# Performance work log

Hardware: AMD Instinct MI355X
Metric: run time of the kernel (lower is better)

The kernel has to match this reference:

```python
import jax, jax.numpy as jnp
import numpy as np

S = 512      # num_seg (queries)
T = 16384    # frames
D = 512      # d_model
DFF = 2048   # dim_feedforward
EPS = 1e-5


def layer_norm(x, g, b):
    mu = jnp.mean(x, axis=-1, keepdims=True)
    var = jnp.mean((x - mu) ** 2, axis=-1, keepdims=True)
    return (x - mu) * jax.lax.rsqrt(var + EPS) * g + b


def setup_inputs() -> dict:
    key = jax.random.key(0)
    ks = jax.random.split(key, 16)
    inv = 1.0 / np.sqrt(D)
    invf = 1.0 / np.sqrt(DFF)
    # action_idx: exactly S contiguous segments over T frames
    action_idx = (jnp.arange(T, dtype=jnp.int32) * S) // T
    return {
        "tgt": jax.random.normal(ks[0], (S, 1, D), jnp.float32),
        "memory": jax.random.normal(ks[1], (T, 1, D), jnp.float32),
        "pos": jax.random.normal(ks[2], (T, 1, D), jnp.float32),
        "query_pos": jax.random.normal(ks[3], (S, 1, D), jnp.float32),
        "action_idx": action_idx,
        "W_tgt2": jax.random.uniform(ks[4], (D, D), jnp.float32, -inv, inv),
        "b_tgt2": jax.random.uniform(ks[5], (D,), jnp.float32, -inv, inv),
        "W1": jax.random.uniform(ks[6], (DFF, D), jnp.float32, -inv, inv),
        "b1": jax.random.uniform(ks[7], (DFF,), jnp.float32, -inv, inv),
        "W2": jax.random.uniform(ks[8], (D, DFF), jnp.float32, -invf, invf),
        "b2": jax.random.uniform(ks[9], (D,), jnp.float32, -invf, invf),
        "g2": jnp.ones((D,), jnp.float32),
        "be2": jnp.zeros((D,), jnp.float32),
        "g3": jnp.ones((D,), jnp.float32),
        "be3": jnp.zeros((D,), jnp.float32),
    }


def reference(tgt, memory, pos, query_pos, action_idx,
              W_tgt2, b_tgt2, W1, b1, W2, b2, g2, be2, g3, be3):
    num_seg, _, dim = tgt.shape
    q = tgt + query_pos          # [S, 1, D]
    k = memory + pos             # [T, 1, D]
    v = memory                   # [T, 1, D]

    # segment-neighbor mask: seg_id per frame; query s attends to frames in
    # segments {s-1, s, s+1}
    change = jnp.concatenate([jnp.zeros((1,), jnp.int32),
                              (action_idx[1:] != action_idx[:-1]).astype(jnp.int32)])
    seg_id = jnp.cumsum(change)                                   # [T]
    mask = jnp.abs(seg_id[None, :] - jnp.arange(num_seg)[:, None]) <= 1  # [S, T]

    scores = jnp.einsum("sbd,tbd->bst", q, k) / np.sqrt(dim)      # [1, S, T]
    scores = jnp.where(mask[None], scores, -jnp.inf)
    attn = jax.nn.softmax(scores, axis=-1)                        # [1, S, T]

    ctx = jnp.einsum("bst,tbd->sbd", attn, v)                     # [S, 1, D]
    tgt2 = jax.nn.relu(ctx) @ W_tgt2.T + b_tgt2                   # [S, 1, D]
    x = layer_norm(tgt + tgt2, g2, be2)
    ffn = jax.nn.relu(x @ W1.T + b1) @ W2.T + b2
    out = layer_norm(x + ffn, g3, be3)
    return out
```

## Files before the change

kernel.cpp:

```cpp
#include <hip/hip_runtime.h>
#include <math.h>

#define S_Q  512
#define T_F  16384
#define D_M  512
#define DFF_ 2048
#define SEG  32

typedef __attribute__((ext_vector_type(8))) short short8;
typedef __attribute__((ext_vector_type(4))) float floatx4;

__device__ __forceinline__ unsigned short f2bf(float f) {
    unsigned int u = __builtin_bit_cast(unsigned int, f);
    u += 0x7FFFu + ((u >> 16) & 1u);
    return (unsigned short)(u >> 16);
}

__device__ __forceinline__ void async_copy16(const void* g, void* l) {
    __builtin_amdgcn_global_load_lds(
        (const __attribute__((address_space(1))) void*)g,
        (__attribute__((address_space(3))) void*)l, 16, 0, 0);
}

__global__ __launch_bounds__(256) void conv3_bf16(
    const float* __restrict__ w0, unsigned short* __restrict__ o0, int n0,
    const float* __restrict__ w1, unsigned short* __restrict__ o1, int n1,
    const float* __restrict__ w2, unsigned short* __restrict__ o2)
{
    int i = (blockIdx.x * 256 + threadIdx.x) * 4;
    const float* src; unsigned short* dst;
    if (i < n0)            { src = w0; dst = o0; }
    else if (i < n0 + n1)  { src = w1; dst = o1; i -= n0; }
    else                   { src = w2; dst = o2; i -= n0 + n1; }
    const float4 v = *(const float4*)(src + i);
    unsigned short o[4] = {f2bf(v.x), f2bf(v.y), f2bf(v.z), f2bf(v.w)};
    *(uint2*)(dst + i) = *(const uint2*)o;
}

__global__ __launch_bounds__(256) void attn_kernel(
    const float* __restrict__ tgt, const float* __restrict__ memory,
    const float* __restrict__ pos, const float* __restrict__ query_pos,
    unsigned short* __restrict__ rc)
{
    const int b    = blockIdx.x;
    const int s    = (b & 7) * 64 + (b >> 3);
    const int tid  = threadIdx.x;
    const int lane = tid & 63;
    const int wave = tid >> 6;

    __shared__ float q[D_M];
    __shared__ float sc[96];

    for (int d = tid; d < D_M; d += 256)
        q[d] = tgt[s * D_M + d] + query_pos[s * D_M + d];
    __syncthreads();

    int lo = (s - 1) * SEG; if (lo < 0) lo = 0;
    int hi = (s + 2) * SEG; if (hi > T_F) hi = T_F;
    const int nf = hi - lo;

    const float4* q4 = (const float4*)q;
    #pragma unroll 2
    for (int f = wave; f < nf; f += 4) {
        const float4* m4 = (const float4*)(memory + (size_t)(lo + f) * D_M);
        const float4* p4 = (const float4*)(pos    + (size_t)(lo + f) * D_M);
        float acc = 0.f;
        #pragma unroll
        for (int j = 0; j < 2; ++j) {
            const int idx = lane + 64 * j;
            const float4 qq = q4[idx], mm = m4[idx], pp = p4[idx];
            acc += qq.x * (mm.x + pp.x) + qq.y * (mm.y + pp.y)
                 + qq.z * (mm.z + pp.z) + qq.w * (mm.w + pp.w);
        }
        #pragma unroll
        for (int off = 32; off > 0; off >>= 1)
            acc += __shfl_xor(acc, off, 64);
        if (lane == 0) sc[f] = acc * 0.04419417382415922f;
    }
    __syncthreads();

    float m = -1e30f;
    for (int f = 0; f < nf; ++f) m = fmaxf(m, sc[f]);
    __syncthreads();
    for (int f = tid; f < nf; f += 256) sc[f] = __expf(sc[f] - m);
    __syncthreads();
    float denom = 0.f;
    for (int f = 0; f < nf; ++f) denom += sc[f];
    const float inv = 1.f / denom;

    float ax = 0.f, ay = 0.f;
    const int d0 = tid * 2;
    #pragma unroll 4
    for (int f = 0; f < nf; ++f) {
        const float a = sc[f];
        const float2 v = *(const float2*)(memory + (size_t)(lo + f) * D_M + d0);
        ax += a * v.x; ay += a * v.y;
    }
    const unsigned short o0 = f2bf(fmaxf(ax * inv, 0.f));
    const unsigned short o1 = f2bf(fmaxf(ay * inv, 0.f));
    *(unsigned int*)(rc + (size_t)s * D_M + d0) = (unsigned int)o0 | ((unsigned int)o1 << 16);
}

template<int BM, bool RELU, bool ADDRES, bool OUT_BF16>
__global__ __launch_bounds__(256) void gemm_mfma(
    const unsigned short* __restrict__ A,
    const unsigned short* __restrict__ B,
    const float* __restrict__ bias,
    const float* __restrict__ res,
    void* __restrict__ Cout, int M, int N, int K)
{
    constexpr int BK = 64;
    constexpr int WT = BM / 2;
    constexpr int NT = WT / 16;
    constexpr int NR = BM / 32;
    __shared__ short As[BM * BK];
    __shared__ short Bs[BM * BK];

    const int tid  = threadIdx.x;
    const int lane = tid & 63;
    const int wave = tid >> 6;
    const int m0 = blockIdx.y * BM;
    const int n0 = blockIdx.x * BM;

    const int srow = tid >> 3;
    const int scol = (tid & 7) * 8;
    const int quad = lane >> 4;
    const int r16  = lane & 15;
    const int wm = (wave >> 1) * WT;
    const int wn = (wave & 1) * WT;

    floatx4 acc[NT][NT] = {};

    for (int k0 = 0; k0 < K; k0 += BK) {
        #pragma unroll
        for (int r = 0; r < NR; ++r) {
            async_copy16(A + (size_t)(m0 + r * 32 + srow) * K + k0 + scol,
                         As + r * 2048 + wave * 512);
            async_copy16(B + (size_t)(n0 + r * 32 + srow) * K + k0 + scol,
                         Bs + r * 2048 + wave * 512);
        }
        __syncthreads();
        #pragma unroll
        for (int ks = 0; ks < 2; ++ks) {
            short8 a[NT], bb[NT];
            #pragma unroll
            for (int i = 0; i < NT; ++i) {
                a[i]  = *(const short8*)(As + (wm + i * 16 + r16) * BK + ks * 32 + quad * 8);
                bb[i] = *(const short8*)(Bs + (wn + i * 16 + r16) * BK + ks * 32 + quad * 8);
            }
            #pragma unroll
            for (int i = 0; i < NT; ++i)
                #pragma unroll
                for (int j = 0; j < NT; ++j)
                    acc[i][j] = __builtin_amdgcn_mfma_f32_16x16x32_bf16(a[i], bb[j], acc[i][j], 0, 0, 0);
        }
        __syncthreads();
    }

    #pragma unroll
    for (int nj = 0; nj < NT; ++nj) {
        const int col = n0 + wn + nj * 16 + r16;
        const float bs = bias[col];
        #pragma unroll
        for (int mi = 0; mi < NT; ++mi) {
            #pragma unroll
            for (int r = 0; r < 4; ++r) {
                const int row = m0 + wm + mi * 16 + quad * 4 + r;
                float c = acc[mi][nj][r] + bs;
                if (RELU)   c = fmaxf(c, 0.f);
                if (ADDRES) c += res[(size_t)row * N + col];
                if (OUT_BF16)
                    ((unsigned short*)Cout)[(size_t)row * N + col] = f2bf(c);
                else
                    ((float*)Cout)[(size_t)row * N + col] = c;
            }
        }
    }
}

template<bool WRITE_BF16>
__global__ __launch_bounds__(256) void ln_kernel(
    const float* __restrict__ X, const float* __restrict__ g,
    const float* __restrict__ be, float* __restrict__ out,
    unsigned short* __restrict__ out_bf)
{
    const int row  = blockIdx.x * 4 + (threadIdx.x >> 6);
    const int lane = threadIdx.x & 63;
    const float* x = X + (size_t)row * D_M;

    float v[8];
    float sum = 0.f;
    #pragma unroll
    for (int j = 0; j < 8; ++j) { v[j] = x[lane + 64 * j]; sum += v[j]; }
    #pragma unroll
    for (int off = 32; off > 0; off >>= 1) sum += __shfl_xor(sum, off, 64);
    const float mu = sum * (1.0f / 512.0f);

    float var = 0.f;
    #pragma unroll
    for (int j = 0; j < 8; ++j) { const float d = v[j] - mu; var += d * d; }
    #pragma unroll
    for (int off = 32; off > 0; off >>= 1) var += __shfl_xor(var, off, 64);
    const float r = rsqrtf(var * (1.0f / 512.0f) + 1e-5f);

    #pragma unroll
    for (int j = 0; j < 8; ++j) {
        const int d = lane + 64 * j;
        const float o = (v[j] - mu) * r * g[d] + be[d];
        out[(size_t)row * D_M + d] = o;
        if (WRITE_BF16) out_bf[(size_t)row * D_M + d] = f2bf(o);
    }
}

extern "C" void kernel_launch(void* const* d_in, const int* in_sizes, int n_in,
                              void* d_out, int out_size, void* d_ws, size_t ws_size,
                              hipStream_t stream) {
    const float* tgt       = (const float*)d_in[0];
    const float* memory    = (const float*)d_in[1];
    const float* pos       = (const float*)d_in[2];
    const float* query_pos = (const float*)d_in[3];
    const float* W_tgt2 = (const float*)d_in[5];
    const float* b_tgt2 = (const float*)d_in[6];
    const float* W1     = (const float*)d_in[7];
    const float* b1     = (const float*)d_in[8];
    const float* W2     = (const float*)d_in[9];
    const float* b2     = (const float*)d_in[10];
    const float* g2     = (const float*)d_in[11];
    const float* be2    = (const float*)d_in[12];
    const float* g3     = (const float*)d_in[13];
    const float* be3    = (const float*)d_in[14];
    float* out = (float*)d_out;

    char* w = (char*)d_ws;
    unsigned short* rc  = (unsigned short*)w;  w += (size_t)S_Q * D_M * 2;
    float* y            = (float*)w;           w += (size_t)S_Q * D_M * 4;
    float* x            = (float*)w;           w += (size_t)S_Q * D_M * 4;
    unsigned short* xb  = (unsigned short*)w;  w += (size_t)S_Q * D_M * 2;
    unsigned short* h   = (unsigned short*)w;  w += (size_t)S_Q * DFF_ * 2;
    float* y2           = (float*)w;           w += (size_t)S_Q * D_M * 4;
    unsigned short* Wt2b= (unsigned short*)w;  w += (size_t)D_M * D_M * 2;
    unsigned short* W1b = (unsigned short*)w;  w += (size_t)DFF_ * D_M * 2;
    unsigned short* W2b = (unsigned short*)w;  w += (size_t)D_M * DFF_ * 2;

    conv3_bf16<<<(D_M * D_M + DFF_ * D_M + D_M * DFF_) / 1024, 256, 0, stream>>>(
        W_tgt2, Wt2b, D_M * D_M, W1, W1b, DFF_ * D_M, W2, W2b);

    attn_kernel<<<S_Q, 256, 0, stream>>>(tgt, memory, pos, query_pos, rc);

    gemm_mfma<32, false, true, false><<<dim3(D_M / 32, S_Q / 32), 256, 0, stream>>>(
        rc, Wt2b, b_tgt2, tgt, y, S_Q, D_M, D_M);
    ln_kernel<true><<<S_Q / 4, 256, 0, stream>>>(y, g2, be2, x, xb);
    gemm_mfma<64, true, false, true><<<dim3(DFF_ / 64, S_Q / 64), 256, 0, stream>>>(
        xb, W1b, b1, nullptr, h, S_Q, DFF_, D_M);
    gemm_mfma<32, false, true, false><<<dim3(D_M / 32, S_Q / 32), 256, 0, stream>>>(
        h, W2b, b2, x, y2, S_Q, D_M, DFF_);
    ln_kernel<false><<<S_Q / 4, 256, 0, stream>>>(y2, g3, be3, out, nullptr);
}
```

Baseline: 192.1 us.

## Restructure attention per segment, add split-K GEMMs, double buffering, fused LN merge

Attention now runs one block per key segment. Each block loads the segment's memory into LDS once and computes partial softmax statistics and context for the three neighbouring queries, so memory and pos are no longer re-read three times. A merge kernel combines the partials with a log-sum-exp rescale. The GEMMs gain double-buffered LDS staging, and the two narrow GEMMs use split-K to expose more blocks. Bias, residual and partial reduction move into the layernorm kernels. The cost is an extra kernel launch and extra workspace traffic for the partials.

```diff
diff --git a/kernel.cpp b/kernel.cpp
--- a/kernel.cpp
+++ b/kernel.cpp
@@ -6,6 +6,7 @@
 #define D_M  512
 #define DFF_ 2048
 #define SEG  32
+#define SCALE 0.04419417382415922f
 
 typedef __attribute__((ext_vector_type(8))) short short8;
 typedef __attribute__((ext_vector_type(4))) float floatx4;
@@ -37,90 +38,166 @@
     *(uint2*)(dst + i) = *(const uint2*)o;
 }
 
-__global__ __launch_bounds__(256) void attn_kernel(
+__global__ __launch_bounds__(256) void attn_seg(
     const float* __restrict__ tgt, const float* __restrict__ memory,
-    const float* __restrict__ pos, const float* __restrict__ query_pos,
-    unsigned short* __restrict__ rc)
-{
-    const int b    = blockIdx.x;
-    const int s    = (b & 7) * 64 + (b >> 3);
+    const float* __restrict__ pos, const float* __restrict__ qp,
+    float* __restrict__ part,
+    float2* __restrict__ me)
+{
+    const int j    = blockIdx.x;
     const int tid  = threadIdx.x;
     const int lane = tid & 63;
     const int wave = tid >> 6;
 
-    __shared__ float q[D_M];
-    __shared__ float sc[96];
-
-    for (int d = tid; d < D_M; d += 256)
-        q[d] = tgt[s * D_M + d] + query_pos[s * D_M + d];
+    __shared__ float v[SEG * D_M];
+    __shared__ float sc[3][SEG];
+    __shared__ float pr[3][SEG];
+
+    {
+        const float* g = memory + (size_t)j * SEG * D_M + (size_t)wave * 16 * 256 + lane * 4;
+        #pragma unroll
+        for (int r = 0; r < 16; ++r)
+            async_copy16(g + r * 256, v + (wave * 16 + r) * 256);
+    }
+
+    float q0[8] = {}, q1[8] = {}, q2[8] = {};
+    {
+        const int d = lane * 8;
+        if (j > 0) {
+            const float4 a0 = *(const float4*)(tgt + (size_t)(j - 1) * D_M + d);
+            const float4 a1 = *(const float4*)(tgt + (size_t)(j - 1) * D_M + d + 4);
+            const float4 b0 = *(const float4*)(qp  + (size_t)(j - 1) * D_M + d);
+            const float4 b1 = *(const float4*)(qp  + (size_t)(j - 1) * D_M + d + 4);
+            q0[0]=a0.x+b0.x; q0[1]=a0.y+b0.y; q0[2]=a0.z+b0.z; q0[3]=a0.w+b0.w;
+            q0[4]=a1.x+b1.x; q0[5]=a1.y+b1.y; q0[6]=a1.z+b1.z; q0[7]=a1.w+b1.w;
+        }
+        {
+            const float4 a0 = *(const float4*)(tgt + (size_t)j * D_M + d);
+            const float4 a1 = *(const float4*)(tgt + (size_t)j * D_M + d + 4);
+            const float4 b0 = *(const float4*)(qp  + (size_t)j * D_M + d);
+            const float4 b1 = *(const float4*)(qp  + (size_t)j * D_M + d + 4);
+            q1[0]=a0.x+b0.x; q1[1]=a0.y+b0.y; q1[2]=a0.z+b0.z; q1[3]=a0.w+b0.w;
+            q1[4]=a1.x+b1.x; q1[5]=a1.y+b1.y; q1[6]=a1.z+b1.z; q1[7]=a1.w+b1.w;
+        }
+        if (j < S_Q - 1) {
+            const float4 a0 = *(const float4*)(tgt + (size_t)(j + 1) * D_M + d);
+            const float4 a1 = *(const float4*)(tgt + (size_t)(j + 1) * D_M + d + 4);
+            const float4 b0 = *(const float4*)(qp  + (size_t)(j + 1) * D_M + d);
+            const float4 b1 = *(const float4*)(qp  + (size_t)(j + 1) * D_M + d + 4);
+            q2[0]=a0.x+b0.x; q2[1]=a0.y+b0.y; q2[2]=a0.z+b0.z; q2[3]=a0.w+b0.w;
+            q2[4]=a1.x+b1.x; q2[5]=a1.y+b1.y; q2[6]=a1.z+b1.z; q2[7]=a1.w+b1.w;
+        }
+    }
     __syncthreads();
 
-    int lo = (s - 1) * SEG; if (lo < 0) lo = 0;
-    int hi = (s + 2) * SEG; if (hi > T_F) hi = T_F;
-    const int nf = hi - lo;
-
-    const float4* q4 = (const float4*)q;
-    #pragma unroll 2
-    for (int f = wave; f < nf; f += 4) {
-        const float4* m4 = (const float4*)(memory + (size_t)(lo + f) * D_M);
-        const float4* p4 = (const float4*)(pos    + (size_t)(lo + f) * D_M);
-        float acc = 0.f;
-        #pragma unroll
-        for (int j = 0; j < 2; ++j) {
-            const int idx = lane + 64 * j;
-            const float4 qq = q4[idx], mm = m4[idx], pp = p4[idx];
-            acc += qq.x * (mm.x + pp.x) + qq.y * (mm.y + pp.y)
-                 + qq.z * (mm.z + pp.z) + qq.w * (mm.w + pp.w);
-        }
-        #pragma unroll
-        for (int off = 32; off > 0; off >>= 1)
-            acc += __shfl_xor(acc, off, 64);
-        if (lane == 0) sc[f] = acc * 0.04419417382415922f;
+    #pragma unroll
+    for (int r = 0; r < 8; ++r) {
+        const int f = wave * 8 + r;
+        const size_t t = (size_t)(j * SEG + f);
+        const float4 pA = *(const float4*)(pos + t * D_M + lane * 8);
+        const float4 pB = *(const float4*)(pos + t * D_M + lane * 8 + 4);
+        const float4 mA = *(const float4*)(v + f * D_M + lane * 8);
+        const float4 mB = *(const float4*)(v + f * D_M + lane * 8 + 4);
+        const float k8[8] = {mA.x+pA.x, mA.y+pA.y, mA.z+pA.z, mA.w+pA.w,
+                             mB.x+pB.x, mB.y+pB.y, mB.z+pB.z, mB.w+pB.w};
+        float a0 = 0.f, a1 = 0.f, a2 = 0.f;
+        #pragma unroll
+        for (int i = 0; i < 8; ++i) {
+            a0 += k8[i] * q0[i]; a1 += k8[i] * q1[i]; a2 += k8[i] * q2[i];
+        }
+        #pragma unroll
+        for (int off = 32; off > 0; off >>= 1) {
+            a0 += __shfl_xor(a0, off, 64);
+            a1 += __shfl_xor(a1, off, 64);
+            a2 += __shfl_xor(a2, off, 64);
+        }
+        if (lane == 0) { sc[0][f] = a0 * SCALE; sc[1][f] = a1 * SCALE; sc[2][f] = a2 * SCALE; }
     }
     __syncthreads();
 
-    float m = -1e30f;
-    for (int f = 0; f < nf; ++f) m = fmaxf(m, sc[f]);
+    if (wave < 3) {
+        float mx = -1e30f;
+        for (int f = 0; f < SEG; ++f) mx = fmaxf(mx, sc[wave][f]);
+        float e = 0.f;
+        for (int f = 0; f < SEG; ++f) {
+            const float pe = __expf(sc[wave][f] - mx);
+            e += pe;
+            if (lane == 0) pr[wave][f] = pe;
+        }
+        const int q = j - 1 + wave;
+        if (lane == 0 && q >= 0 && q < S_Q)
+            me[q * 3 + (2 - wave)] = make_float2(mx, e);
+    }
     __syncthreads();
-    for (int f = tid; f < nf; f += 256) sc[f] = __expf(sc[f] - m);
-    __syncthreads();
-    float denom = 0.f;
-    for (int f = 0; f < nf; ++f) denom += sc[f];
-    const float inv = 1.f / denom;
-
-    float ax = 0.f, ay = 0.f;
+
     const int d0 = tid * 2;
-    #pragma unroll 4
-    for (int f = 0; f < nf; ++f) {
-        const float a = sc[f];
-        const float2 v = *(const float2*)(memory + (size_t)(lo + f) * D_M + d0);
-        ax += a * v.x; ay += a * v.y;
-    }
-    const unsigned short o0 = f2bf(fmaxf(ax * inv, 0.f));
-    const unsigned short o1 = f2bf(fmaxf(ay * inv, 0.f));
-    *(unsigned int*)(rc + (size_t)s * D_M + d0) = (unsigned int)o0 | ((unsigned int)o1 << 16);
-}
-
-template<int BM, bool RELU, bool ADDRES, bool OUT_BF16>
+    float c0x=0,c0y=0,c1x=0,c1y=0,c2x=0,c2y=0;
+    for (int f = 0; f < SEG; ++f) {
+        const float2 vv = *(const float2*)(v + f * D_M + d0);
+        const float w0 = pr[0][f], w1 = pr[1][f], w2 = pr[2][f];
+        c0x += w0 * vv.x; c0y += w0 * vv.y;
+        c1x += w1 * vv.x; c1y += w1 * vv.y;
+        c2x += w2 * vv.x; c2y += w2 * vv.y;
+    }
+    if (j > 0)
+        *(float2*)(part + ((size_t)(j - 1) * 3 + 2) * D_M + d0) = make_float2(c0x, c0y);
+    *(float2*)(part + ((size_t)j * 3 + 1) * D_M + d0) = make_float2(c1x, c1y);
+    if (j < S_Q - 1)
+        *(float2*)(part + ((size_t)(j + 1) * 3 + 0) * D_M + d0) = make_float2(c2x, c2y);
+}
+
+__global__ __launch_bounds__(256) void attn_merge(
+    const float* __restrict__ part, const float2* __restrict__ me,
+    unsigned short* __restrict__ rc)
+{
+    const int row  = blockIdx.x * 4 + (threadIdx.x >> 6);
+    const int lane = threadIdx.x & 63;
+    const int slo = (row == 0)       ? 1 : 0;
+    const int shi = (row == S_Q - 1) ? 1 : 2;
+
+    float mx = -1e30f;
+    for (int s = slo; s <= shi; ++s) mx = fmaxf(mx, me[row * 3 + s].x);
+    float den = 0.f, c[3] = {0.f, 0.f, 0.f};
+    for (int s = slo; s <= shi; ++s) {
+        c[s] = __expf(me[row * 3 + s].x - mx);
+        den += me[row * 3 + s].y * c[s];
+    }
+    const float inv = 1.f / den;
+
+    const int d = lane * 8;
+    float acc[8] = {};
+    for (int s = slo; s <= shi; ++s) {
+        const float4 a = *(const float4*)(part + ((size_t)row * 3 + s) * D_M + d);
+        const float4 b = *(const float4*)(part + ((size_t)row * 3 + s) * D_M + d + 4);
+        acc[0]+=c[s]*a.x; acc[1]+=c[s]*a.y; acc[2]+=c[s]*a.z; acc[3]+=c[s]*a.w;
+        acc[4]+=c[s]*b.x; acc[5]+=c[s]*b.y; acc[6]+=c[s]*b.z; acc[7]+=c[s]*b.w;
+    }
+    unsigned short o[8];
+    #pragma unroll
+    for (int i = 0; i < 8; ++i) o[i] = f2bf(fmaxf(acc[i] * inv, 0.f));
+    *(uint4*)(rc + (size_t)row * D_M + d) = *(const uint4*)o;
+}
+
+template<int BM, int KSPLIT, bool RELU, bool ADDRES, bool OUT_BF16>
 __global__ __launch_bounds__(256) void gemm_mfma(
-    const unsigned short* __restrict__ A,
-    const unsigned short* __restrict__ B,
-    const float* __restrict__ bias,
-    const float* __restrict__ res,
+    const unsigned short* __restrict__ A, const unsigned short* __restrict__ B,
+    const float* __restrict__ bias, const float* __restrict__ res,
     void* __restrict__ Cout, int M, int N, int K)
 {
     constexpr int BK = 64;
     constexpr int WT = BM / 2;
     constexpr int NT = WT / 16;
     constexpr int NR = BM / 32;
-    __shared__ short As[BM * BK];
-    __shared__ short Bs[BM * BK];
+    __shared__ short As[2][BM * BK];
+    __shared__ short Bs[2][BM * BK];
 
     const int tid  = threadIdx.x;
     const int lane = tid & 63;
     const int wave = tid >> 6;
     const int m0 = blockIdx.y * BM;
     const int n0 = blockIdx.x * BM;
+    const int kbase = (K / KSPLIT) * blockIdx.z;
+    const int niter = (K / KSPLIT) / BK;
 
     const int srow = tid >> 3;
     const int scol = (tid & 7) * 8;
@@ -131,84 +208,121 @@
 
     floatx4 acc[NT][NT] = {};
 
-    for (int k0 = 0; k0 < K; k0 += BK) {
-        #pragma unroll
-        for (int r = 0; r < NR; ++r) {
-            async_copy16(A + (size_t)(m0 + r * 32 + srow) * K + k0 + scol,
-                         As + r * 2048 + wave * 512);
-            async_copy16(B + (size_t)(n0 + r * 32 + srow) * K + k0 + scol,
-                         Bs + r * 2048 + wave * 512);
-        }
+    #pragma unroll
+    for (int r = 0; r < NR; ++r) {
+        async_copy16(A + (size_t)(m0 + r * 32 + srow) * K + kbase + scol, &As[0][r * 2048 + wave * 512]);
+        async_copy16(B + (size_t)(n0 + r * 32 + srow) * K + kbase + scol, &Bs[0][r * 2048 + wave * 512]);
+    }
+
+    for (int it = 0; it < niter; ++it) {
         __syncthreads();
+        if (it + 1 < niter) {
+            const int k0 = kbase + (it + 1) * BK;
+            const int nb = (it + 1) & 1;
+            #pragma unroll
+            for (int r = 0; r < NR; ++r) {
+                async_copy16(A + (size_t)(m0 + r * 32 + srow) * K + k0 + scol, &As[nb][r * 2048 + wave * 512]);
+                async_copy16(B + (size_t)(n0 + r * 32 + srow) * K + k0 + scol, &Bs[nb][r * 2048 + wave * 512]);
+            }
+        }
+        const short* Ab = As[it & 1];
+        const short* Bb = Bs[it & 1];
         #pragma unroll
         for (int ks = 0; ks < 2; ++ks) {
             short8 a[NT], bb[NT];
             #pragma unroll
             for (int i = 0; i < NT; ++i) {
-                a[i]  = *(const short8*)(As + (wm + i * 16 + r16) * BK + ks * 32 + quad * 8);
-                bb[i] = *(const short8*)(Bs + (wn + i * 16 + r16) * BK + ks * 32 + quad * 8);
+                a[i]  = *(const short8*)(Ab + (wm + i * 16 + r16) * BK + ks * 32 + quad * 8);
+                bb[i] = *(const short8*)(Bb + (wn + i * 16 + r16) * BK + ks * 32 + quad * 8);
             }
             #pragma unroll
             for (int i = 0; i < NT; ++i)
                 #pragma unroll
-                for (int j = 0; j < NT; ++j)
-                    acc[i][j] = __builtin_amdgcn_mfma_f32_16x16x32_bf16(a[i], bb[j], acc[i][j], 0, 0, 0);
-        }
-        __syncthreads();
+                for (int jn = 0; jn < NT; ++jn)
+                    acc[i][jn] = __builtin_amdgcn_mfma_f32_16x16x32_bf16(a[i], bb[jn], acc[i][jn], 0, 0, 0);
+        }
     }
 
     #pragma unroll
     for (int nj = 0; nj < NT; ++nj) {
         const int col = n0 + wn + nj * 16 + r16;
-        const float bs = bias[col];
         #pragma unroll
         for (int mi = 0; mi < NT; ++mi) {
             #pragma unroll
             for (int r = 0; r < 4; ++r) {
                 const int row = m0 + wm + mi * 16 + quad * 4 + r;
-                float c = acc[mi][nj][r] + bs;
-                if (RELU)   c = fmaxf(c, 0.f);
-                if (ADDRES) c += res[(size_t)row * N + col];
-                if (OUT_BF16)
-                    ((unsigned short*)Cout)[(size_t)row * N + col] = f2bf(c);
-                else
-                    ((float*)Cout)[(size_t)row * N + col] = c;
+                float cv = acc[mi][nj][r];
+                if (KSPLIT > 1) {
+                    ((float*)Cout)[((size_t)blockIdx.z * M + row) * N + col] = cv;
+                } else {
+                    cv += bias[col];
+                    if (RELU)   cv = fmaxf(cv, 0.f);
+                    if (ADDRES) cv += res[(size_t)row * N + col];
+                    if (OUT_BF16)
+                        ((unsigned short*)Cout)[(size_t)row * N + col] = f2bf(cv);
+                    else
+                        ((float*)Cout)[(size_t)row * N + col] = cv;
+                }
             }
         }
     }
 }
 
-template<bool WRITE_BF16>
-__global__ __launch_bounds__(256) void ln_kernel(
-    const float* __restrict__ X, const float* __restrict__ g,
-    const float* __restrict__ be, float* __restrict__ out,
-    unsigned short* __restrict__ out_bf)
+template<int NP, bool WRITE_BF16>
+__global__ __launch_bounds__(256) void ln_merge(
+    const float* __restrict__ parts,
+    const float* __restrict__ res, const float* __restrict__ bias,
+    const float* __restrict__ g, const float* __restrict__ be,
+    float* __restrict__ out, unsigned short* __restrict__ out_bf)
 {
     const int row  = blockIdx.x * 4 + (threadIdx.x >> 6);
     const int lane = threadIdx.x & 63;
-    const float* x = X + (size_t)row * D_M;
-
-    float v[8];
+
+    float vv[8];
+    #pragma unroll
+    for (int hh = 0; hh < 2; ++hh) {
+        const int d = lane * 8 + hh * 4;
+        float4 a = *(const float4*)(res + (size_t)row * D_M + d);
+        const float4 b = *(const float4*)(bias + d);
+        a.x += b.x; a.y += b.y; a.z += b.z; a.w += b.w;
+        #pragma unroll
+        for (int z = 0; z < NP; ++z) {
+            const float4 p = *(const float4*)(parts + ((size_t)z * S_Q + row) * D_M + d);
+            a.x += p.x; a.y += p.y; a.z += p.z; a.w += p.w;
+        }
+        vv[hh * 4 + 0] = a.x; vv[hh * 4 + 1] = a.y;
+        vv[hh * 4 + 2] = a.z; vv[hh * 4 + 3] = a.w;
+    }
+
     float sum = 0.f;
     #pragma unroll
-    for (int j = 0; j < 8; ++j) { v[j] = x[lane + 64 * j]; sum += v[j]; }
+    for (int i = 0; i < 8; ++i) sum += vv[i];
     #pragma unroll
     for (int off = 32; off > 0; off >>= 1) sum += __shfl_xor(sum, off, 64);
     const float mu = sum * (1.0f / 512.0f);
 
     float var = 0.f;
     #pragma unroll
-    for (int j = 0; j < 8; ++j) { const float d = v[j] - mu; var += d * d; }
+    for (int i = 0; i < 8; ++i) { const float dd = vv[i] - mu; var += dd * dd; }
     #pragma unroll
     for (int off = 32; off > 0; off >>= 1) var += __shfl_xor(var, off, 64);
-    const float r = rsqrtf(var * (1.0f / 512.0f) + 1e-5f);
-
-    #pragma unroll
-    for (int j = 0; j < 8; ++j) {
-        const int d = lane + 64 * j;
-        const float o = (v[j] - mu) * r * g[d] + be[d];
-        out[(size_t)row * D_M + d] = o;
-        if (WRITE_BF16) out_bf[(size_t)row * D_M + d] = f2bf(o);
+    const float rr = rsqrtf(var * (1.0f / 512.0f) + 1e-5f);
+
+    #pragma unroll
+    for (int hh = 0; hh < 2; ++hh) {
+        const int d = lane * 8 + hh * 4;
+        const float4 gg = *(const float4*)(g + d);
+        const float4 bb = *(const float4*)(be + d);
+        float4 o;
+        o.x = (vv[hh*4+0] - mu) * rr * gg.x + bb.x;
+        o.y = (vv[hh*4+1] - mu) * rr * gg.y + bb.y;
+        o.z = (vv[hh*4+2] - mu) * rr * gg.z + bb.z;
+        o.w = (vv[hh*4+3] - mu) * rr * gg.w + bb.w;
+        *(float4*)(out + (size_t)row * D_M + d) = o;
+        if (WRITE_BF16) {
+            unsigned short ob[4] = {f2bf(o.x), f2bf(o.y), f2bf(o.z), f2bf(o.w)};
+            *(uint2*)(out_bf + (size_t)row * D_M + d) = *(const uint2*)ob;
+        }
     }
 }
 
@@ -232,27 +346,33 @@
     float* out = (float*)d_out;
 
     char* w = (char*)d_ws;
-    unsigned short* rc  = (unsigned short*)w;  w += (size_t)S_Q * D_M * 2;
-    float* y            = (float*)w;           w += (size_t)S_Q * D_M * 4;
-    float* x            = (float*)w;           w += (size_t)S_Q * D_M * 4;
-    unsigned short* xb  = (unsigned short*)w;  w += (size_t)S_Q * D_M * 2;
-    unsigned short* h   = (unsigned short*)w;  w += (size_t)S_Q * DFF_ * 2;
-    float* y2           = (float*)w;           w += (size_t)S_Q * D_M * 4;
-    unsigned short* Wt2b= (unsigned short*)w;  w += (size_t)D_M * D_M * 2;
-    unsigned short* W1b = (unsigned short*)w;  w += (size_t)DFF_ * D_M * 2;
-    unsigned short* W2b = (unsigned short*)w;  w += (size_t)D_M * DFF_ * 2;
+    float* part   = (float*)w;
+    float* gpart1 = (float*)(w + 3145728);
+    float* gpart3 = (float*)w;
+    size_t off = 5242880;
+    float2* me          = (float2*)(w + off);          off += 12288;
+    unsigned short* rc  = (unsigned short*)(w + off);  off += 524288;
+    float* x            = (float*)(w + off);           off += 1048576;
+    unsigned short* xb  = (unsigned short*)(w + off);  off += 524288;
+    unsigned short* h   = (unsigned short*)(w + off);  off += 2097152;
+    unsigned short* Wt2b= (unsigned short*)(w + off);  off += 524288;
+    unsigned short* W1b = (unsigned short*)(w + off);  off += 2097152;
+    unsigned short* W2b = (unsigned short*)(w + off);  off += 2097152;
 
     conv3_bf16<<<(D_M * D_M + DFF_ * D_M + D_M * DFF_) / 1024, 256, 0, stream>>>(
         W_tgt2, Wt2b, D_M * D_M, W1, W1b, DFF_ * D_M, W2, W2b);
 
-    attn_kernel<<<S_Q, 256, 0, stream>>>(tgt, memory, pos, query_pos, rc);
-
-    gemm_mfma<32, false, true, false><<<dim3(D_M / 32, S_Q / 32), 256, 0, stream>>>(
-        rc, Wt2b, b_tgt2, tgt, y, S_Q, D_M, D_M);
-    ln_kernel<true><<<S_Q / 4, 256, 0, stream>>>(y, g2, be2, x, xb);
-    gemm_mfma<64, true, false, true><<<dim3(DFF_ / 64, S_Q / 64), 256, 0, stream>>>(
+    attn_seg<<<S_Q, 256, 0, stream>>>(tgt, memory, pos, query_pos, part, me);
+    attn_merge<<<S_Q / 4, 256, 0, stream>>>(part, me, rc);
+
+    gemm_mfma<32, 2, false, false, false><<<dim3(16, 16, 2), 256, 0, stream>>>(
+        rc, Wt2b, nullptr, nullptr, gpart1, S_Q, D_M, D_M);
+    ln_merge<2, true><<<S_Q / 4, 256, 0, stream>>>(
+        gpart1, tgt, b_tgt2, g2, be2, x, xb);
+    gemm_mfma<64, 1, true, false, true><<<dim3(DFF_ / 64, S_Q / 64, 1), 256, 0, stream>>>(
         xb, W1b, b1, nullptr, h, S_Q, DFF_, D_M);
-    gemm_mfma<32, false, true, false><<<dim3(D_M / 32, S_Q / 32), 256, 0, stream>>>(
-        h, W2b, b2, x, y2, S_Q, D_M, DFF_);
-    ln_kernel<false><<<S_Q / 4, 256, 0, stream>>>(y2, g3, be3, out, nullptr);
-}
+    gemm_mfma<32, 4, false, false, false><<<dim3(16, 16, 4), 256, 0, stream>>>(
+        h, W2b, nullptr, nullptr, gpart3, S_Q, D_M, DFF_);
+    ln_merge<4, false><<<S_Q / 4, 256, 0, stream>>>(
+        gpart3, x, b2, g3, be3, out, nullptr);
+}
```

After: 163.2 us. 15.1% less time.
